# Kernel tuning notes

Hardware: AMD Instinct MI355X
Metric: run time of the kernel (lower is better)

## Reference

```python
import jax, jax.numpy as jnp
import numpy as np

DIM = 4096
N_HEADS = 32
N_KV_HEADS = 8
HEAD_DIM = 128
SEQ = 2048
REPEATS = N_HEADS // N_KV_HEADS
SCALE = HEAD_DIM ** -0.5


def setup_inputs() -> dict:
    key = jax.random.key(0)
    ks = jax.random.split(key, 7)
    x = jax.random.normal(ks[0], (SEQ, DIM), dtype=jnp.float32)
    # rotary freqs_cis = exp(i * pos * theta^(-2j/d)) -> cos/sin, shape (S, head_dim/2)
    theta = 10000.0
    inv_freq = 1.0 / (theta ** (np.arange(0, HEAD_DIM, 2, dtype=np.float32) / HEAD_DIM))
    ang = np.arange(SEQ, dtype=np.float32)[:, None] * inv_freq[None, :]
    freqs_cos = jnp.asarray(np.cos(ang), dtype=jnp.float32)
    freqs_sin = jnp.asarray(np.sin(ang), dtype=jnp.float32)
    s = 0.02
    wq = s * jax.random.normal(ks[1], (DIM, N_HEADS * HEAD_DIM), dtype=jnp.float32)
    wk = s * jax.random.normal(ks[2], (DIM, N_KV_HEADS * HEAD_DIM), dtype=jnp.float32)
    wv = s * jax.random.normal(ks[3], (DIM, N_KV_HEADS * HEAD_DIM), dtype=jnp.float32)
    wo = s * jax.random.normal(ks[4], (N_HEADS * HEAD_DIM, DIM), dtype=jnp.float32)
    return {"x": x, "freqs_cos": freqs_cos, "freqs_sin": freqs_sin,
            "wq": wq, "wk": wk, "wv": wv, "wo": wo}


def _rope(t, cos, sin):
    # t: (S, H, D); treat last dim as D/2 complex pairs and rotate by freqs_cis
    S, H, D = t.shape
    tr = t.reshape(S, H, D // 2, 2)
    t1, t2 = tr[..., 0], tr[..., 1]
    c = cos[:, None, :]  # (S, 1, D/2)
    s = sin[:, None, :]
    o1 = t1 * c - t2 * s
    o2 = t1 * s + t2 * c
    return jnp.stack([o1, o2], axis=-1).reshape(S, H, D)


def reference(x, freqs_cos, freqs_sin, wq, wk, wv, wo):
    S = x.shape[0]
    xq = (x @ wq).reshape(S, N_HEADS, HEAD_DIM)
    xk = (x @ wk).reshape(S, N_KV_HEADS, HEAD_DIM)
    xv = (x @ wv).reshape(S, N_KV_HEADS, HEAD_DIM)
    xq = _rope(xq, freqs_cos, freqs_sin)
    xk = _rope(xk, freqs_cos, freqs_sin)
    # cache=None path: key,val = xk,xv; repeat_kv via repeat_interleave on head dim
    key = jnp.repeat(xk, REPEATS, axis=1)  # (S, H, D)
    val = jnp.repeat(xv, REPEATS, axis=1)
    # scaled dot-product attention, mask=None (cache is None)
    scores = jnp.einsum('qhd,khd->hqk', xq, key) * SCALE  # (H, S, S)
    att = jax.nn.softmax(scores, axis=-1)
    out = jnp.einsum('hqk,khd->qhd', att, val)  # (S, H, D)
    out = out.reshape(S, N_HEADS * HEAD_DIM)
    return out @ wo
```

## Files before the change

kernel.cpp:

```cpp
#include <hip/hip_runtime.h>
#include <hip/hip_bf16.h>

#define SEQ   2048
#define DIM   4096
#define NH    32
#define NKV   8
#define HD    128
#define KVDIM 1024
#define SCALE 0.08838834764831845f

typedef __attribute__((ext_vector_type(8))) short bf16x8;
typedef __attribute__((ext_vector_type(4))) float f32x4;
typedef __attribute__((ext_vector_type(16))) float f32x16;

__device__ __forceinline__ ushort f2bf(float f) {
  __hip_bfloat16 h = __float2bfloat16(f);
  return *reinterpret_cast<ushort*>(&h);
}

typedef const __attribute__((address_space(1))) uint* gas_ptr;
typedef __attribute__((address_space(3))) uint* las_ptr;
__device__ __forceinline__ void async16(const ushort* g, ushort* l) {
  __builtin_amdgcn_global_load_lds((gas_ptr)g, (las_ptr)l, 16, 0, 0);
}

__device__ __forceinline__ uint cvtpk(float lo, float hi) {
  uint r;
  asm("v_cvt_pk_bf16_f32 %0, %1, %2" : "=v"(r) : "v"(lo), "v"(hi));
  return r;
}
__device__ __forceinline__ void plswap(uint& a, uint& b) {
  asm("v_permlane32_swap_b32 %0, %1" : "+v"(a), "+v"(b));
}

__global__ __launch_bounds__(256) void convert_f32_bf16(
    const float* __restrict__ in, ushort* __restrict__ out)
{
  int i = (blockIdx.x * 256 + threadIdx.x) * 8;
  float4 a = *(const float4*)(in + i);
  float4 b = *(const float4*)(in + i + 4);
  uint4 u;
  u.x = (uint)f2bf(a.x) | ((uint)f2bf(a.y) << 16);
  u.y = (uint)f2bf(a.z) | ((uint)f2bf(a.w) << 16);
  u.z = (uint)f2bf(b.x) | ((uint)f2bf(b.y) << 16);
  u.w = (uint)f2bf(b.z) | ((uint)f2bf(b.w) << 16);
  *(uint4*)(out + i) = u;
}

__global__ __launch_bounds__(256) void transpose_w(
    const float* __restrict__ W, ushort* __restrict__ WT, int K, int N)
{
  __shared__ float t[32][33];
  const int k0 = blockIdx.y * 32, n0 = blockIdx.x * 32;
  const int tid = threadIdx.x;
  {
    int r = tid >> 3, c0 = (tid & 7) * 4;
    float4 v = *(const float4*)(W + (size_t)(k0 + r) * N + n0 + c0);
    t[r][c0] = v.x; t[r][c0 + 1] = v.y; t[r][c0 + 2] = v.z; t[r][c0 + 3] = v.w;
  }
  __syncthreads();
  {
    int n = tid >> 3, kc = (tid & 7) * 4;
    ushort4 u;
    u.x = f2bf(t[kc + 0][n]); u.y = f2bf(t[kc + 1][n]);
    u.z = f2bf(t[kc + 2][n]); u.w = f2bf(t[kc + 3][n]);
    *(ushort4*)(WT + (size_t)(n0 + n) * K + k0 + kc) = u;
  }
}

__global__ __launch_bounds__(256) void gemm_bt(
    const ushort* __restrict__ A, const ushort* __restrict__ BT,
    void* __restrict__ Cv, void* __restrict__ C2v,
    int M, int N, int K, int mode)
{
  __shared__ __align__(16) ushort As[128 * 64];
  __shared__ __align__(16) ushort Bs[128 * 64];

  const int tid  = threadIdx.x;
  const int lane = tid & 63;
  const int w    = tid >> 6;
  const int wr = w >> 1, wc = w & 1;
  const int quad = lane >> 4, l16 = lane & 15;
  const int m0 = blockIdx.y * 128, n0 = blockIdx.x * 128;
  const int srow8 = lane >> 3;
  const int sswz  = ((lane & 7) ^ srow8) << 3;

  f32x4 acc[4][4];
#pragma unroll
  for (int bm = 0; bm < 4; ++bm)
#pragma unroll
    for (int bn = 0; bn < 4; ++bn)
      acc[bm][bn] = (f32x4){0.f, 0.f, 0.f, 0.f};

  for (int k0 = 0; k0 < K; k0 += 64) {
#pragma unroll
    for (int j = 0; j < 4; ++j) {
      const int rb = w * 32 + j * 8;
      async16(A  + (size_t)(m0 + rb + srow8) * K + k0 + sswz, &As[rb * 64]);
      async16(BT + (size_t)(n0 + rb + srow8) * K + k0 + sswz, &Bs[rb * 64]);
    }
    __syncthreads();

#pragma unroll
    for (int s = 0; s < 2; ++s) {
      bf16x8 af[4], bf[4];
#pragma unroll
      for (int bm = 0; bm < 4; ++bm) {
        const int row = wr * 64 + bm * 16 + l16;
        af[bm] = *(const bf16x8*)&As[row * 64 + (((s * 4 + quad) ^ (row & 7)) << 3)];
      }
#pragma unroll
      for (int bn = 0; bn < 4; ++bn) {
        const int row = wc * 64 + bn * 16 + l16;
        bf[bn] = *(const bf16x8*)&Bs[row * 64 + (((s * 4 + quad) ^ (row & 7)) << 3)];
      }
#pragma unroll
      for (int bm = 0; bm < 4; ++bm)
#pragma unroll
        for (int bn = 0; bn < 4; ++bn)
          acc[bm][bn] = __builtin_amdgcn_mfma_f32_16x16x32_bf16(
              af[bm], bf[bn], acc[bm][bn], 0, 0, 0);
    }
    __syncthreads();
  }

  if (mode == 0) {
    ushort* C = (ushort*)Cv;
#pragma unroll
    for (int bm = 0; bm < 4; ++bm) {
      int rbase = m0 + wr * 64 + bm * 16 + quad * 4;
#pragma unroll
      for (int bn = 0; bn < 4; ++bn) {
        int col = n0 + wc * 64 + bn * 16 + l16;
#pragma unroll
        for (int i = 0; i < 4; ++i)
          C[(size_t)(rbase + i) * N + col] = f2bf(acc[bm][bn][i]);
      }
    }
  } else if (mode == 1) {
    float* C = (float*)Cv;
#pragma unroll
    for (int bm = 0; bm < 4; ++bm) {
      int rbase = m0 + wr * 64 + bm * 16 + quad * 4;
#pragma unroll
      for (int bn = 0; bn < 4; ++bn) {
        int col = n0 + wc * 64 + bn * 16 + l16;
#pragma unroll
        for (int i = 0; i < 4; ++i)
          C[(size_t)(rbase + i) * N + col] = acc[bm][bn][i];
      }
    }
  } else {
    if (n0 < 4096) {
      ushort* C = (ushort*)Cv;
#pragma unroll
      for (int bm = 0; bm < 4; ++bm) {
        int rbase = m0 + wr * 64 + bm * 16 + quad * 4;
#pragma unroll
        for (int bn = 0; bn < 4; ++bn) {
          int col = n0 + wc * 64 + bn * 16 + l16;
#pragma unroll
          for (int i = 0; i < 4; ++i)
            C[(size_t)(rbase + i) * DIM + col] = f2bf(acc[bm][bn][i]);
        }
      }
    } else if (n0 < 5120) {
      ushort* C = (ushort*)C2v;
#pragma unroll
      for (int bm = 0; bm < 4; ++bm) {
        int rbase = m0 + wr * 64 + bm * 16 + quad * 4;
#pragma unroll
        for (int bn = 0; bn < 4; ++bn) {
          int col = n0 + wc * 64 + bn * 16 + l16 - 4096;
#pragma unroll
          for (int i = 0; i < 4; ++i)
            C[(size_t)(rbase + i) * KVDIM + col] = f2bf(acc[bm][bn][i]);
        }
      }
    } else {
      ushort* C2 = (ushort*)C2v + (size_t)SEQ * KVDIM;
#pragma unroll
      for (int bm = 0; bm < 4; ++bm) {
        int rbase = m0 + wr * 64 + bm * 16 + quad * 4;
#pragma unroll
        for (int bn = 0; bn < 4; ++bn) {
          int col = n0 + wc * 64 + bn * 16 + l16 - 5120;
          ushort4 u;
          u.x = f2bf(acc[bm][bn][0]); u.y = f2bf(acc[bm][bn][1]);
          u.z = f2bf(acc[bm][bn][2]); u.w = f2bf(acc[bm][bn][3]);
          *(ushort4*)(C2 + (size_t)col * SEQ + rbase) = u;
        }
      }
    }
  }
}

__device__ __forceinline__ float bfhi(uint u) {
  union { uint i; float f; } v; v.i = u & 0xffff0000u; return v.f;
}
__device__ __forceinline__ float bflo(uint u) {
  union { uint i; float f; } v; v.i = u << 16; return v.f;
}
__global__ __launch_bounds__(256) void rope_kernel(
    ushort* __restrict__ t, const float* __restrict__ cosb,
    const float* __restrict__ sinb, int shift)
{
  int idx = blockIdx.x * 256 + threadIdx.x;
  int p  = idx & 63;
  int sh = idx >> 6;
  int s  = sh >> shift;
  uint* bp = (uint*)(t + ((size_t)sh << 7)) + p;
  uint u = *bp;
  float t1 = bflo(u), t2 = bfhi(u);
  float c  = cosb[(s << 6) + p];
  float sv = sinb[(s << 6) + p];
  float o1 = t1 * c - t2 * sv;
  float o2 = t1 * sv + t2 * c;
  *bp = ((uint)f2bf(o1)) | (((uint)f2bf(o2)) << 16);
}

#define OFF_V0U 8192
#define OFF_V1U 16384
#define NT (SEQ / 64)

__device__ __forceinline__ void stage_K(const ushort* __restrict__ K, ushort* SM,
                                        int w, int lane, int kb, int kvh) {
  const int r4 = lane >> 4, c16 = lane & 15;
#pragma unroll
  for (int j = 0; j < 4; ++j) {
    int rb = w * 16 + j * 4, row = rb + r4;
    int c = c16 ^ (row & 15);
    async16(K + (size_t)(kb + row) * KVDIM + kvh * HD + c * 8, &SM[rb * 128]);
  }
}
__device__ __forceinline__ void stage_V(const ushort* __restrict__ VT, ushort* SMv,
                                        int w, int lane, int kb, int kvh) {
  const int r8 = lane >> 3, c8 = lane & 7;
#pragma unroll
  for (int j = 0; j < 4; ++j) {
    int rb = w * 32 + j * 8, row = rb + r8;
    int c = c8 ^ (row & 7);
    async16(VT + (size_t)(kvh * 128 + row) * SEQ + kb + c * 8, &SMv[rb * 64]);
  }
}

__global__ __launch_bounds__(256, 2) void attn_mfma5(
    const ushort* __restrict__ Q, const ushort* __restrict__ K,
    const ushort* __restrict__ VT, ushort* __restrict__ O)
{
  __shared__ __align__(16) ushort SM[24576];

  const int tid = threadIdx.x, lane = tid & 63, w = tid >> 6;
  const int l31 = lane & 31, hi = lane >> 5;
  const int kx = l31 & 15;
  const int vx = lane & 7;
  const int h = blockIdx.y, kvh = h >> 2;
  const int q0 = blockIdx.x * 128;

  {
    const int r4 = lane >> 4, c16 = lane & 15;
#pragma unroll
    for (int j = 0; j < 8; ++j) {
      int rb = w * 32 + j * 4, row = rb + r4;
      int c = c16 ^ (row & 15);
      async16(Q + (size_t)(q0 + row) * DIM + h * HD + c * 8, &SM[rb * 128]);
    }
  }
  __syncthreads();

  bf16x8 qf[8];
#pragma unroll
  for (int ks = 0; ks < 8; ++ks) {
    int cc = ((2 * ks + hi) ^ kx) << 3;
    qf[ks] = *(const bf16x8*)&SM[(w * 32 + l31) * 128 + cc];
  }
  __syncthreads();

  stage_K(K, SM, w, lane, 0, kvh);
  stage_V(VT, &SM[OFF_V0U], w, lane, 0, kvh);

  f32x16 oacc[4];
#pragma unroll
  for (int dt = 0; dt < 4; ++dt)
#pragma unroll
    for (int r = 0; r < 16; ++r) oacc[dt][r] = 0.f;
  float m_i = -1e30f, l_i = 0.f;

  for (int t = 0; t < NT; ++t) {
    __syncthreads();

    f32x16 s0, s1;
#pragma unroll
    for (int r = 0; r < 16; ++r) { s0[r] = 0.f; s1[r] = 0.f; }
    __builtin_amdgcn_s_setprio(1);
#pragma unroll
    for (int ks = 0; ks < 8; ++ks) {
      int cc = ((2 * ks + hi) ^ kx) << 3;
      bf16x8 k0 = *(const bf16x8*)&SM[l31 * 128 + cc];
      bf16x8 k1 = *(const bf16x8*)&SM[(32 + l31) * 128 + cc];
      s0 = __builtin_amdgcn_mfma_f32_32x32x16_bf16(k0, qf[ks], s0, 0, 0, 0);
      s1 = __builtin_amdgcn_mfma_f32_32x32x16_bf16(k1, qf[ks], s1, 0, 0, 0);
    }
    __builtin_amdgcn_s_setprio(0);

    __syncthreads();

    if (t + 1 < NT) {
      stage_K(K, SM, w, lane, (t + 1) * 64, kvh);
      stage_V(VT, &SM[((t + 1) & 1) ? OFF_V1U : OFF_V0U], w, lane, (t + 1) * 64, kvh);
    }

    float tm[16];
#pragma unroll
    for (int i = 0; i < 16; ++i) tm[i] = fmaxf(s0[i], s1[i]);
#pragma unroll
    for (int d = 8; d >= 1; d >>= 1)
#pragma unroll
      for (int i = 0; i < 8; ++i) if (i < d) tm[i] = fmaxf(tm[i], tm[i + d]);
    float lm = fmaxf(tm[0], __shfl_xor(tm[0], 32));
    float lmS = lm * SCALE;
    float mn;
    if (__any(lmS > m_i + 8.0f)) {
      mn = fmaxf(m_i, lmS);
      float al = __expf(m_i - mn);
      m_i = mn; l_i *= al;
#pragma unroll
      for (int dt = 0; dt < 4; ++dt)
#pragma unroll
        for (int r = 0; r < 16; ++r) oacc[dt][r] *= al;
    } else mn = m_i;

    float p0[16], p1[16];
#pragma unroll
    for (int r = 0; r < 16; ++r) p0[r] = __expf(fmaf(s0[r], SCALE, -mn));
#pragma unroll
    for (int r = 0; r < 16; ++r) p1[r] = __expf(fmaf(s1[r], SCALE, -mn));
    {
      float ts[16];
#pragma unroll
      for (int i = 0; i < 16; ++i) ts[i] = p0[i] + p1[i];
#pragma unroll
      for (int d = 8; d >= 1; d >>= 1)
#pragma unroll
        for (int i = 0; i < 8; ++i) if (i < d) ts[i] += ts[i + d];
      l_i += ts[0] + __shfl_xor(ts[0], 32);
    }

    bf16x8 pf[4];
    {
      uint a0 = cvtpk(p0[0], p0[1]),  b0 = cvtpk(p0[4], p0[5]);   plswap(a0, b0);
      uint a1 = cvtpk(p0[2], p0[3]),  b1 = cvtpk(p0[6], p0[7]);   plswap(a1, b1);
      uint4 u0 = {a0, a1, b0, b1};  pf[0] = *(bf16x8*)&u0;
      uint a2 = cvtpk(p0[8], p0[9]),  b2 = cvtpk(p0[12], p0[13]); plswap(a2, b2);
      uint a3 = cvtpk(p0[10], p0[11]),b3 = cvtpk(p0[14], p0[15]); plswap(a3, b3);
      uint4 u1 = {a2, a3, b2, b3};  pf[1] = *(bf16x8*)&u1;
      uint a4 = cvtpk(p1[0], p1[1]),  b4 = cvtpk(p1[4], p1[5]);   plswap(a4, b4);
      uint a5 = cvtpk(p1[2], p1[3]),  b5 = cvtpk(p1[6], p1[7]);   plswap(a5, b5);
      uint4 u2 = {a4, a5, b4, b5};  pf[2] = *(bf16x8*)&u2;
      uint a6 = cvtpk(p1[8], p1[9]),  b6 = cvtpk(p1[12], p1[13]); plswap(a6, b6);
      uint a7 = cvtpk(p1[10], p1[11]),b7 = cvtpk(p1[14], p1[15]); plswap(a7, b7);
      uint4 u3 = {a6, a7, b6, b7};  pf[3] = *(bf16x8*)&u3;
    }

    const int vbU = (t & 1) ? OFF_V1U : OFF_V0U;
    __builtin_amdgcn_s_setprio(1);
#pragma unroll
    for (int ks = 0; ks < 4; ++ks) {
      int cc = ((2 * ks + hi) ^ vx) << 3;
#pragma unroll
      for (int dt = 0; dt < 4; ++dt) {
        bf16x8 vf = *(const bf16x8*)&SM[vbU + (dt * 32 + l31) * 64 + cc];
        oacc[dt] = __builtin_amdgcn_mfma_f32_32x32x16_bf16(vf, pf[ks], oacc[dt], 0, 0, 0);
      }
    }
    __builtin_amdgcn_s_setprio(0);
  }

  float linv = 1.0f / l_i;
  const int RB = w * 4096;
#pragma unroll
  for (int dt = 0; dt < 4; ++dt)
#pragma unroll
    for (int r = 0; r < 16; ++r) {
      int d = dt * 32 + (r & 3) + 8 * (r >> 2) + 4 * hi;
      SM[RB + l31 * 128 + (((d >> 3) ^ (l31 & 15)) << 3) + (d & 7)] =
          f2bf(oacc[dt][r] * linv);
    }
  {
    const int r4 = lane >> 4, c16 = lane & 15;
#pragma unroll
    for (int i = 0; i < 8; ++i) {
      int qq = i * 4 + r4;
      uint4 v = *(const uint4*)&SM[RB + qq * 128 + ((c16 ^ (qq & 15)) << 3)];
      *(uint4*)(O + (size_t)(q0 + w * 32 + qq) * DIM + h * HD + c16 * 8) = v;
    }
  }
}

extern "C" void kernel_launch(void* const* d_in, const int* in_sizes, int n_in,
                              void* d_out, int out_size, void* d_ws, size_t ws_size,
                              hipStream_t stream) {
  const float* x  = (const float*)d_in[0];
  const float* fc = (const float*)d_in[1];
  const float* fs = (const float*)d_in[2];
  const float* wq = (const float*)d_in[3];
  const float* wk = (const float*)d_in[4];
  const float* wv = (const float*)d_in[5];
  const float* wo = (const float*)d_in[6];
  float* out = (float*)d_out;

  ushort* xb   = (ushort*)d_ws;
  ushort* wT   = xb   + (size_t)SEQ * DIM;
  ushort* wkvT = wT   + (size_t)DIM * DIM;
  ushort* qb   = wkvT + (size_t)2048 * DIM;
  ushort* kb   = qb   + (size_t)SEQ * DIM;
  ushort* vT   = kb   + (size_t)SEQ * KVDIM;
  ushort* ab   = qb;

  dim3 blk(256);

  convert_f32_bf16<<<(SEQ * DIM) / 2048, blk, 0, stream>>>(x, xb);
  transpose_w<<<dim3(DIM / 32, DIM / 32), blk, 0, stream>>>(wq, wT, DIM, DIM);
  transpose_w<<<dim3(KVDIM / 32, DIM / 32), blk, 0, stream>>>(wk, wkvT, DIM, KVDIM);
  transpose_w<<<dim3(KVDIM / 32, DIM / 32), blk, 0, stream>>>(wv, wkvT + (size_t)KVDIM * DIM, DIM, KVDIM);

  gemm_bt<<<dim3(6144 / 128, SEQ / 128), blk, 0, stream>>>(xb, wT, qb, kb, SEQ, 6144, DIM, 2);

  rope_kernel<<<(SEQ * NH * 64) / 256, blk, 0, stream>>>(qb, fc, fs, 5);
  rope_kernel<<<(SEQ * NKV * 64) / 256, blk, 0, stream>>>(kb, fc, fs, 3);

  attn_mfma5<<<dim3(SEQ / 128, NH), blk, 0, stream>>>(qb, kb, vT, ab);

  transpose_w<<<dim3(DIM / 32, DIM / 32), blk, 0, stream>>>(wo, wT, DIM, DIM);
  gemm_bt<<<dim3(DIM / 128, SEQ / 128), blk, 0, stream>>>(ab, wT, out, nullptr, SEQ, DIM, DIM, 1);
}
```

Before: 540.5 us.

## Triple-buffer GEMM LDS tiles with async prefetch two k-steps ahead

Replaces the single-buffered 64-wide k-tile GEMM loop with a 3-stage ring of 32-wide k-tiles. Loads for tile t+2 are issued with global_load_lds while tile t is computed, using vmcnt waits and a single barrier per iteration. MFMA issue is wrapped in raised wave priority. This targets exposed global-load latency and the two barriers per iteration, at the cost of smaller k-steps, more loop iterations, and reliance on hand-counted vmcnt correctness.

```diff
diff --git a/kernel.cpp b/kernel.cpp
--- a/kernel.cpp
+++ b/kernel.cpp
@@ -68,13 +68,29 @@
   }
 }
 
+__device__ __forceinline__ void stage_tile(
+    const ushort* __restrict__ A, const ushort* __restrict__ BT,
+    ushort* as, ushort* bs, int m0, int n0, int K, int k0, int w, int lane)
+{
+  const int rl = lane >> 2;
+  const int cl = lane & 3;
+#pragma unroll
+  for (int i = 0; i < 2; ++i) {
+    const int rb = i * 64 + w * 16;
+    const int r  = rb + rl;
+    const int sc = (cl ^ (r & 3)) << 3;
+    async16(A  + (size_t)(m0 + r) * K + k0 + sc, as + rb * 32);
+    async16(BT + (size_t)(n0 + r) * K + k0 + sc, bs + rb * 32);
+  }
+}
+
 __global__ __launch_bounds__(256) void gemm_bt(
     const ushort* __restrict__ A, const ushort* __restrict__ BT,
     void* __restrict__ Cv, void* __restrict__ C2v,
     int M, int N, int K, int mode)
 {
-  __shared__ __align__(16) ushort As[128 * 64];
-  __shared__ __align__(16) ushort Bs[128 * 64];
+  __shared__ __align__(16) ushort As[3][128 * 32];
+  __shared__ __align__(16) ushort Bs[3][128 * 32];
 
   const int tid  = threadIdx.x;
   const int lane = tid & 63;
@@ -82,8 +98,6 @@
   const int wr = w >> 1, wc = w & 1;
   const int quad = lane >> 4, l16 = lane & 15;
   const int m0 = blockIdx.y * 128, n0 = blockIdx.x * 128;
-  const int srow8 = lane >> 3;
-  const int sswz  = ((lane & 7) ^ srow8) << 3;
 
   f32x4 acc[4][4];
 #pragma unroll
@@ -92,36 +106,43 @@
     for (int bn = 0; bn < 4; ++bn)
       acc[bm][bn] = (f32x4){0.f, 0.f, 0.f, 0.f};
 
-  for (int k0 = 0; k0 < K; k0 += 64) {
-#pragma unroll
-    for (int j = 0; j < 4; ++j) {
-      const int rb = w * 32 + j * 8;
-      async16(A  + (size_t)(m0 + rb + srow8) * K + k0 + sswz, &As[rb * 64]);
-      async16(BT + (size_t)(n0 + rb + srow8) * K + k0 + sswz, &Bs[rb * 64]);
-    }
-    __syncthreads();
-
-#pragma unroll
-    for (int s = 0; s < 2; ++s) {
-      bf16x8 af[4], bf[4];
-#pragma unroll
-      for (int bm = 0; bm < 4; ++bm) {
-        const int row = wr * 64 + bm * 16 + l16;
-        af[bm] = *(const bf16x8*)&As[row * 64 + (((s * 4 + quad) ^ (row & 7)) << 3)];
-      }
-#pragma unroll
-      for (int bn = 0; bn < 4; ++bn) {
-        const int row = wc * 64 + bn * 16 + l16;
-        bf[bn] = *(const bf16x8*)&Bs[row * 64 + (((s * 4 + quad) ^ (row & 7)) << 3)];
-      }
-#pragma unroll
-      for (int bm = 0; bm < 4; ++bm)
-#pragma unroll
-        for (int bn = 0; bn < 4; ++bn)
-          acc[bm][bn] = __builtin_amdgcn_mfma_f32_16x16x32_bf16(
-              af[bm], bf[bn], acc[bm][bn], 0, 0, 0);
-    }
-    __syncthreads();
+  const int nt = K >> 5;
+  stage_tile(A, BT, As[0], Bs[0], m0, n0, K, 0, w, lane);
+  stage_tile(A, BT, As[1], Bs[1], m0, n0, K, 32, w, lane);
+
+  for (int t = 0; t < nt; ++t) {
+    if (t + 1 < nt) {
+      asm volatile("s_waitcnt vmcnt(4)" ::: "memory");
+    } else {
+      asm volatile("s_waitcnt vmcnt(0)" ::: "memory");
+    }
+    __builtin_amdgcn_s_barrier();
+    asm volatile("" ::: "memory");
+    if (t + 2 < nt)
+      stage_tile(A, BT, As[(t + 2) % 3], Bs[(t + 2) % 3],
+                 m0, n0, K, (t + 2) * 32, w, lane);
+
+    const ushort* as = As[t % 3];
+    const ushort* bs = Bs[t % 3];
+    bf16x8 af[4], bf[4];
+#pragma unroll
+    for (int bm = 0; bm < 4; ++bm) {
+      const int row = wr * 64 + bm * 16 + l16;
+      af[bm] = *(const bf16x8*)&as[row * 32 + ((quad ^ (row & 3)) << 3)];
+    }
+#pragma unroll
+    for (int bn = 0; bn < 4; ++bn) {
+      const int row = wc * 64 + bn * 16 + l16;
+      bf[bn] = *(const bf16x8*)&bs[row * 32 + ((quad ^ (row & 3)) << 3)];
+    }
+    __builtin_amdgcn_s_setprio(1);
+#pragma unroll
+    for (int bm = 0; bm < 4; ++bm)
+#pragma unroll
+      for (int bn = 0; bn < 4; ++bn)
+        acc[bm][bn] = __builtin_amdgcn_mfma_f32_16x16x32_bf16(
+            af[bm], bf[bn], acc[bm][bn], 0, 0, 0);
+    __builtin_amdgcn_s_setprio(0);
   }
 
   if (mode == 0) {
```

New measurement: 538.2 us. No clear change (-0.4%).
